# Optimization experiments

Hardware: AMD Instinct MI355X
Metric: run time of the kernel (lower is better)

The kernel has to match this reference:

```python
import jax, jax.numpy as jnp
import numpy as np
import math

B, NH, SQ, HD = 4, 32, 512, 128
MLEN = 3584


def setup_inputs() -> dict:
    key = jax.random.key(0)
    k1, k2, k3, k4 = jax.random.split(key, 4)
    q = jax.random.normal(k1, (B, NH, SQ, HD), dtype=jnp.float32)
    k = jax.random.normal(k2, (B, NH, SQ, HD), dtype=jnp.float32)
    v = jax.random.normal(k3, (B, NH, SQ, HD), dtype=jnp.float32)
    mem = jax.random.normal(k4, (B, MLEN, 2 * NH * HD), dtype=jnp.float32)
    mask = jnp.ones((B, 1, SQ, MLEN + SQ), dtype=jnp.float32)
    return {"q": q, "k": k, "v": v, "mask": mask, "mem": mem}


def reference(q, k, v, mask, mem):
    b, nh, sq, hd = k.shape
    mlen = mem.shape[1]
    # cache_kv: stack (k,v) -> (2,b,nh,sq,hd), permute -> (b,sq,2,nh,hd), flatten
    cache_kv = jnp.stack((k, v)).transpose(1, 3, 0, 2, 4).reshape(b, sq, 2 * nh * hd)
    # split cached mem into memk/memv: (b,mlen,2,nh,hd) -> (2,b,nh,mlen,hd)
    mem_r = mem.reshape(b, mlen, 2, nh, hd).transpose(2, 0, 3, 1, 4)
    k_full = jnp.concatenate([mem_r[0], k], axis=2)  # [b,nh,mlen+sq,hd]
    v_full = jnp.concatenate([mem_r[1], v], axis=2)
    scale = 1.0 / math.sqrt(hd)
    scores = jnp.einsum("bhqd,bhkd->bhqk", q * scale, k_full)
    # standard_attention general mask path (mask.shape[-2] != 1)
    scores = scores * mask - 10000.0 * (1.0 - mask)
    probs = jax.nn.softmax(scores, axis=-1)
    context = jnp.einsum("bhqk,bhkd->bhqd", probs, v_full)
    return context, cache_kv
```

## Files before the change

### kernel.cpp

```cpp
#include <hip/hip_runtime.h>

#define B_ 4
#define NH_ 32
#define SQ_ 512
#define HD_ 128
#define MLEN_ 3584
#define KT_ 4096
#define QB_ 256
#define KB_ 64
#define NTILE_ 64
#define MEMTILES_ 56

typedef float f32x4 __attribute__((ext_vector_type(4)));
typedef short s16x8 __attribute__((ext_vector_type(8)));

__device__ __forceinline__ f32x4 MFMA16(s16x8 a, s16x8 b, f32x4 c) {
    return __builtin_amdgcn_mfma_f32_16x16x32_bf16(a, b, c, 0, 0, 0);
}

__device__ __forceinline__ s16x8 cvt8(float4 a, float4 b, float sc) {
    union { s16x8 v; __bf16 h[8]; } u;
    u.h[0] = (__bf16)(a.x * sc); u.h[1] = (__bf16)(a.y * sc);
    u.h[2] = (__bf16)(a.z * sc); u.h[3] = (__bf16)(a.w * sc);
    u.h[4] = (__bf16)(b.x * sc); u.h[5] = (__bf16)(b.y * sc);
    u.h[6] = (__bf16)(b.z * sc); u.h[7] = (__bf16)(b.w * sc);
    return u.v;
}

__launch_bounds__(512, 2)
__global__ void attn_kernel(const float* __restrict__ q, const float* __restrict__ k,
                            const float* __restrict__ v, const float* __restrict__ mask,
                            const float* __restrict__ mem, float* __restrict__ ctx)
{
    __shared__ __bf16 Klds[KB_ * HD_];
    __shared__ __bf16 Vt[HD_ * KB_];
    __shared__ __bf16 Plds[8 * 32 * KB_];

    const int tid  = threadIdx.x;
    const int lane = tid & 63;
    const int w    = tid >> 6;
    const int l15  = lane & 15;
    const int l4   = lane >> 4;
    const int xv   = (lane & 7) << 4;

    const int qt   = blockIdx.x >> 7;
    const int pair = blockIdx.x & 127;
    const int b    = pair >> 5;
    const int h    = pair & 31;
    const int q0   = qt * QB_;

    const float scale = 0.088388347648318447f;
    s16x8 qf[2][4];
    {
        const float* qbase = q + (((size_t)(b * NH_ + h)) * SQ_ + q0 + w * 32 + l15) * HD_;
        #pragma unroll
        for (int m = 0; m < 2; ++m) {
            #pragma unroll
            for (int kc = 0; kc < 4; ++kc) {
                const float* p = qbase + (size_t)m * 16 * HD_ + kc * 32 + l4 * 8;
                float4 a = *(const float4*)p;
                float4 c = *(const float4*)(p + 4);
                qf[m][kc] = cvt8(a, c, scale);
            }
        }
    }

    f32x4 acc[2][8];
    #pragma unroll
    for (int m = 0; m < 2; ++m)
        #pragma unroll
        for (int n = 0; n < 8; ++n)
            acc[m][n] = (f32x4){0.f, 0.f, 0.f, 0.f};

    float mrun[2][4], lrun[2][4];
    #pragma unroll
    for (int m = 0; m < 2; ++m)
        #pragma unroll
        for (int i = 0; i < 4; ++i) { mrun[m][i] = -3.0e38f; lrun[m][i] = 0.f; }

    const float* maskbase = mask + ((size_t)b * SQ_ + q0 + w * 32 + l4 * 4) * KT_;

    for (int t = 0; t < NTILE_; ++t) {
        const int kv0 = t * KB_;
        const float *srcK, *srcV;
        int rstride;
        if (t < MEMTILES_) {
            const float* mrow = mem + ((size_t)b * MLEN_ + kv0) * (2 * NH_ * HD_) + h * HD_;
            srcK = mrow;
            srcV = mrow + NH_ * HD_;
            rstride = 2 * NH_ * HD_;
        } else {
            size_t off = (((size_t)b * NH_ + h) * SQ_ + (kv0 - MLEN_)) * HD_;
            srcK = k + off;
            srcV = v + off;
            rstride = HD_;
        }

        __syncthreads();

        #pragma unroll
        for (int it = 0; it < 2; ++it) {
            int idx = tid + it * 512;
            int row = idx >> 4, cg = idx & 15;
            const float* p = srcK + (size_t)row * rstride + cg * 8;
            float4 a = *(const float4*)p;
            float4 c = *(const float4*)(p + 4);
            s16x8 vv = cvt8(a, c, 1.0f);
            int byte = row * 256 + ((cg * 16) ^ ((row & 7) << 4));
            *(s16x8*)((char*)Klds + byte) = vv;
        }
        #pragma unroll
        for (int it = 0; it < 2; ++it) {
            int idx = tid + it * 512;
            int hd = idx & 127, kvb = idx >> 7;
            const float* p = srcV + (size_t)(kvb * 8) * rstride + hd;
            union { s16x8 v; __bf16 hh[8]; } u;
            #pragma unroll
            for (int j = 0; j < 8; ++j) u.hh[j] = (__bf16)p[(size_t)j * rstride];
            int byte = hd * 128 + ((kvb * 16) ^ ((hd & 7) << 4));
            *(s16x8*)((char*)Vt + byte) = u.v;
        }

        __syncthreads();

        f32x4 sa[2][4];
        #pragma unroll
        for (int m = 0; m < 2; ++m)
            #pragma unroll
            for (int n = 0; n < 4; ++n)
                sa[m][n] = (f32x4){0.f, 0.f, 0.f, 0.f};
        #pragma unroll
        for (int n = 0; n < 4; ++n) {
            #pragma unroll
            for (int kc = 0; kc < 4; ++kc) {
                s16x8 kf = *(const s16x8*)((const char*)Klds +
                            (n * 16 + l15) * 256 + (((kc * 4 + l4) * 16) ^ xv));
                sa[0][n] = MFMA16(qf[0][kc], kf, sa[0][n]);
                sa[1][n] = MFMA16(qf[1][kc], kf, sa[1][n]);
            }
        }

        #pragma unroll
        for (int m = 0; m < 2; ++m) {
            #pragma unroll
            for (int i = 0; i < 4; ++i) {
                const float* mp = maskbase + (size_t)(m * 16 + i) * KT_ + kv0 + l15;
                float mv0 = mp[0], mv1 = mp[16], mv2 = mp[32], mv3 = mp[48];
                sa[m][0][i] = fmaf(mv0, sa[m][0][i] + 10000.f, -10000.f);
                sa[m][1][i] = fmaf(mv1, sa[m][1][i] + 10000.f, -10000.f);
                sa[m][2][i] = fmaf(mv2, sa[m][2][i] + 10000.f, -10000.f);
                sa[m][3][i] = fmaf(mv3, sa[m][3][i] + 10000.f, -10000.f);

                float rm = fmaxf(fmaxf(sa[m][0][i], sa[m][1][i]),
                                 fmaxf(sa[m][2][i], sa[m][3][i]));
                rm = fmaxf(rm, __shfl_xor(rm, 1));
                rm = fmaxf(rm, __shfl_xor(rm, 2));
                rm = fmaxf(rm, __shfl_xor(rm, 4));
                rm = fmaxf(rm, __shfl_xor(rm, 8));

                float om = mrun[m][i];
                float nm = fmaxf(om, rm);
                float al = __expf(om - nm);
                mrun[m][i] = nm;

                float rs = 0.f;
                #pragma unroll
                for (int n = 0; n < 4; ++n) {
                    float pe = __expf(sa[m][n][i] - nm);
                    sa[m][n][i] = pe;
                    rs += pe;
                }
                rs += __shfl_xor(rs, 1);
                rs += __shfl_xor(rs, 2);
                rs += __shfl_xor(rs, 4);
                rs += __shfl_xor(rs, 8);
                lrun[m][i] = lrun[m][i] * al + rs;

                #pragma unroll
                for (int nn = 0; nn < 8; ++nn) acc[m][nn][i] *= al;
            }
        }

        __bf16* pw = &Plds[w * (32 * KB_)];
        #pragma unroll
        for (int m = 0; m < 2; ++m)
            #pragma unroll
            for (int n = 0; n < 4; ++n)
                #pragma unroll
                for (int i = 0; i < 4; ++i) {
                    int row = m * 16 + l4 * 4 + i;
                    int col = n * 16 + l15;
                    int byte = row * 128 + ((col * 2) ^ ((row & 7) << 4));
                    *(__bf16*)((char*)pw + byte) = (__bf16)sa[m][n][i];
                }

        s16x8 pf[2][2];
        #pragma unroll
        for (int m = 0; m < 2; ++m)
            #pragma unroll
            for (int kt = 0; kt < 2; ++kt)
                pf[m][kt] = *(const s16x8*)((const char*)pw +
                              (m * 16 + l15) * 128 + ((kt * 64 + l4 * 16) ^ xv));
        #pragma unroll
        for (int nn = 0; nn < 8; ++nn) {
            s16x8 vf0 = *(const s16x8*)((const char*)Vt +
                          (nn * 16 + l15) * 128 + ((l4 * 16) ^ xv));
            s16x8 vf1 = *(const s16x8*)((const char*)Vt +
                          (nn * 16 + l15) * 128 + ((64 + l4 * 16) ^ xv));
            #pragma unroll
            for (int m = 0; m < 2; ++m) {
                acc[m][nn] = MFMA16(pf[m][0], vf0, acc[m][nn]);
                acc[m][nn] = MFMA16(pf[m][1], vf1, acc[m][nn]);
            }
        }
    }

    float* obase = ctx + (((size_t)(b * NH_ + h)) * SQ_ + q0 + w * 32 + l4 * 4) * HD_ + l15;
    #pragma unroll
    for (int m = 0; m < 2; ++m)
        #pragma unroll
        for (int i = 0; i < 4; ++i) {
            float inv = 1.f / lrun[m][i];
            #pragma unroll
            for (int nn = 0; nn < 8; ++nn)
                obase[(size_t)(m * 16 + i) * HD_ + nn * 16] = acc[m][nn][i] * inv;
        }
}

__global__ void cachekv_kernel(const float* __restrict__ k, const float* __restrict__ v,
                               float* __restrict__ out)
{
    size_t i = ((size_t)blockIdx.x * 256 + threadIdx.x) * 4;
    unsigned f = (unsigned)i;
    unsigned d    = f & 127;
    unsigned hh   = (f >> 7) & 31;
    unsigned part = (f >> 12) & 1;
    unsigned s    = (f >> 13) & 511;
    unsigned bb   = f >> 22;
    const float* src = (part ? v : k) + (((size_t)(bb * 32u + hh)) * 512u + s) * 128u + d;
    *(float4*)(out + i) = *(const float4*)src;
}

extern "C" void kernel_launch(void* const* d_in, const int* in_sizes, int n_in,
                              void* d_out, int out_size, void* d_ws, size_t ws_size,
                              hipStream_t stream) {
    const float* q    = (const float*)d_in[0];
    const float* k    = (const float*)d_in[1];
    const float* v    = (const float*)d_in[2];
    const float* mask = (const float*)d_in[3];
    const float* mem  = (const float*)d_in[4];
    float* out = (float*)d_out;

    attn_kernel<<<dim3(B_ * NH_ * (SQ_ / QB_)), dim3(512), 0, stream>>>(q, k, v, mask, mem, out);

    const int ctx_elems = B_ * NH_ * SQ_ * HD_;
    const int ckv_elems = B_ * SQ_ * 2 * NH_ * HD_;
    cachekv_kernel<<<dim3(ckv_elems / 4 / 256), dim3(256), 0, stream>>>(k, v, out + ctx_elems);
    (void)in_sizes; (void)n_in; (void)out_size; (void)d_ws; (void)ws_size;
}
```

Measured before the change: 382.9 us.

## Software-pipeline K/V tile loads into registers and prefetch mask values

Global loads for the next K/V tile are issued into registers before computing the current tile, and converted and written to LDS after the compute with an extra barrier. Mask values for the current tile are also loaded at the top of the iteration. The aim is to hide global memory latency behind the MFMA and softmax work. The cost is higher register pressure (about 40 more floats per thread plus mask prefetch), which could reduce occupancy or cause spills.

Result: slower. 409.4 us (+6.9%).

```diff
diff --git a/kernel.cpp b/kernel.cpp
--- a/kernel.cpp
+++ b/kernel.cpp
@@ -80,7 +80,13 @@
 
     const float* maskbase = mask + ((size_t)b * SQ_ + q0 + w * 32 + l4 * 4) * KT_;
 
-    for (int t = 0; t < NTILE_; ++t) {
+    const int krow = tid >> 4,  kcg  = tid & 15;
+    const int vhd  = tid & 127, vkvb = tid >> 7;
+
+    float4 kpa[2], kpb[2];
+    float  vpre[2][8];
+
+    auto issueKV = [&](int t) {
         const int kv0 = t * KB_;
         const float *srcK, *srcV;
         int rstride;
@@ -95,31 +101,55 @@
             srcV = v + off;
             rstride = HD_;
         }
-
-        __syncthreads();
-
-        #pragma unroll
-        for (int it = 0; it < 2; ++it) {
-            int idx = tid + it * 512;
-            int row = idx >> 4, cg = idx & 15;
-            const float* p = srcK + (size_t)row * rstride + cg * 8;
-            float4 a = *(const float4*)p;
-            float4 c = *(const float4*)(p + 4);
-            s16x8 vv = cvt8(a, c, 1.0f);
-            int byte = row * 256 + ((cg * 16) ^ ((row & 7) << 4));
+        #pragma unroll
+        for (int it = 0; it < 2; ++it) {
+            const float* p = srcK + (size_t)(krow + it * 32) * rstride + kcg * 8;
+            kpa[it] = *(const float4*)p;
+            kpb[it] = *(const float4*)(p + 4);
+        }
+        #pragma unroll
+        for (int it = 0; it < 2; ++it) {
+            const float* p = srcV + (size_t)((vkvb + it * 4) * 8) * rstride + vhd;
+            #pragma unroll
+            for (int j = 0; j < 8; ++j) vpre[it][j] = p[(size_t)j * rstride];
+        }
+    };
+    auto writeKV = [&]() {
+        #pragma unroll
+        for (int it = 0; it < 2; ++it) {
+            int row = krow + it * 32;
+            s16x8 vv = cvt8(kpa[it], kpb[it], 1.0f);
+            int byte = row * 256 + ((kcg * 16) ^ ((row & 7) << 4));
             *(s16x8*)((char*)Klds + byte) = vv;
         }
         #pragma unroll
         for (int it = 0; it < 2; ++it) {
-            int idx = tid + it * 512;
-            int hd = idx & 127, kvb = idx >> 7;
-            const float* p = srcV + (size_t)(kvb * 8) * rstride + hd;
+            int kvb = vkvb + it * 4;
             union { s16x8 v; __bf16 hh[8]; } u;
             #pragma unroll
-            for (int j = 0; j < 8; ++j) u.hh[j] = (__bf16)p[(size_t)j * rstride];
-            int byte = hd * 128 + ((kvb * 16) ^ ((hd & 7) << 4));
+            for (int j = 0; j < 8; ++j) u.hh[j] = (__bf16)vpre[it][j];
+            int byte = vhd * 128 + ((kvb * 16) ^ ((vhd & 7) << 4));
             *(s16x8*)((char*)Vt + byte) = u.v;
         }
+    };
+
+    issueKV(0);
+    writeKV();
+
+    for (int t = 0; t < NTILE_; ++t) {
+        const int kv0 = t * KB_;
+
+        float mpre[2][4][4];
+        #pragma unroll
+        for (int m = 0; m < 2; ++m)
+            #pragma unroll
+            for (int i = 0; i < 4; ++i) {
+                const float* mp = maskbase + (size_t)(m * 16 + i) * KT_ + kv0 + l15;
+                #pragma unroll
+                for (int n = 0; n < 4; ++n) mpre[m][i][n] = mp[n * 16];
+            }
+
+        if (t + 1 < NTILE_) issueKV(t + 1);
 
         __syncthreads();
 
@@ -144,12 +174,10 @@
         for (int m = 0; m < 2; ++m) {
             #pragma unroll
             for (int i = 0; i < 4; ++i) {
-                const float* mp = maskbase + (size_t)(m * 16 + i) * KT_ + kv0 + l15;
-                float mv0 = mp[0], mv1 = mp[16], mv2 = mp[32], mv3 = mp[48];
-                sa[m][0][i] = fmaf(mv0, sa[m][0][i] + 10000.f, -10000.f);
-                sa[m][1][i] = fmaf(mv1, sa[m][1][i] + 10000.f, -10000.f);
-                sa[m][2][i] = fmaf(mv2, sa[m][2][i] + 10000.f, -10000.f);
-                sa[m][3][i] = fmaf(mv3, sa[m][3][i] + 10000.f, -10000.f);
+                sa[m][0][i] = fmaf(mpre[m][i][0], sa[m][0][i] + 10000.f, -10000.f);
+                sa[m][1][i] = fmaf(mpre[m][i][1], sa[m][1][i] + 10000.f, -10000.f);
+                sa[m][2][i] = fmaf(mpre[m][i][2], sa[m][2][i] + 10000.f, -10000.f);
+                sa[m][3][i] = fmaf(mpre[m][i][3], sa[m][3][i] + 10000.f, -10000.f);
 
                 float rm = fmaxf(fmaxf(sa[m][0][i], sa[m][1][i]),
                                  fmaxf(sa[m][2][i], sa[m][3][i]));
@@ -213,6 +241,10 @@
                 acc[m][nn] = MFMA16(pf[m][1], vf1, acc[m][nn]);
             }
         }
+
+        __syncthreads();
+
+        if (t + 1 < NTILE_) writeKV();
     }
 
     float* obase = ctx + (((size_t)(b * NH_ + h)) * SQ_ + q0 + w * 32 + l4 * 4) * HD_ + l15;
```

## Halve query tile per block, raise occupancy, and prefetch mask before barrier

Applied to the files above, without the earlier changes.

Cuts the query tile from 256 to 128 rows, so each wave owns 16 query rows instead of 32. This halves the per-thread accumulator, softmax-state and Q-fragment registers and allows 4 blocks per CU. Mask values for a tile are now loaded before the barrier so their latency overlaps the K/V staging. The cost is that every K/V tile, including the large mem cache, is converted and staged by twice as many blocks, which doubles global K/V reads unless L2 or the last-level cache absorbs them.

After: 346.3 us. -9.5%, faster.

```diff
diff --git a/kernel.cpp b/kernel.cpp
--- a/kernel.cpp
+++ b/kernel.cpp
@@ -6,7 +6,7 @@
 #define HD_ 128
 #define MLEN_ 3584
 #define KT_ 4096
-#define QB_ 256
+#define QB_ 128
 #define KB_ 64
 #define NTILE_ 64
 #define MEMTILES_ 56
@@ -18,23 +18,23 @@
     return __builtin_amdgcn_mfma_f32_16x16x32_bf16(a, b, c, 0, 0, 0);
 }
 
-__device__ __forceinline__ s16x8 cvt8(float4 a, float4 b, float sc) {
+__device__ __forceinline__ s16x8 cvt8(float4 a, float4 b) {
     union { s16x8 v; __bf16 h[8]; } u;
-    u.h[0] = (__bf16)(a.x * sc); u.h[1] = (__bf16)(a.y * sc);
-    u.h[2] = (__bf16)(a.z * sc); u.h[3] = (__bf16)(a.w * sc);
-    u.h[4] = (__bf16)(b.x * sc); u.h[5] = (__bf16)(b.y * sc);
-    u.h[6] = (__bf16)(b.z * sc); u.h[7] = (__bf16)(b.w * sc);
+    u.h[0] = (__bf16)a.x; u.h[1] = (__bf16)a.y;
+    u.h[2] = (__bf16)a.z; u.h[3] = (__bf16)a.w;
+    u.h[4] = (__bf16)b.x; u.h[5] = (__bf16)b.y;
+    u.h[6] = (__bf16)b.z; u.h[7] = (__bf16)b.w;
     return u.v;
 }
 
-__launch_bounds__(512, 2)
+__launch_bounds__(512, 4)
 __global__ void attn_kernel(const float* __restrict__ q, const float* __restrict__ k,
                             const float* __restrict__ v, const float* __restrict__ mask,
                             const float* __restrict__ mem, float* __restrict__ ctx)
 {
     __shared__ __bf16 Klds[KB_ * HD_];
     __shared__ __bf16 Vt[HD_ * KB_];
-    __shared__ __bf16 Plds[8 * 32 * KB_];
+    __shared__ __bf16 Plds[8 * 16 * KB_];
 
     const int tid  = threadIdx.x;
     const int lane = tid & 63;
@@ -50,35 +50,29 @@
     const int q0   = qt * QB_;
 
     const float scale = 0.088388347648318447f;
-    s16x8 qf[2][4];
+    s16x8 qf[4];
     {
-        const float* qbase = q + (((size_t)(b * NH_ + h)) * SQ_ + q0 + w * 32 + l15) * HD_;
-        #pragma unroll
-        for (int m = 0; m < 2; ++m) {
-            #pragma unroll
-            for (int kc = 0; kc < 4; ++kc) {
-                const float* p = qbase + (size_t)m * 16 * HD_ + kc * 32 + l4 * 8;
-                float4 a = *(const float4*)p;
-                float4 c = *(const float4*)(p + 4);
-                qf[m][kc] = cvt8(a, c, scale);
-            }
+        const float* qbase = q + (((size_t)(b * NH_ + h)) * SQ_ + q0 + w * 16 + l15) * HD_;
+        #pragma unroll
+        for (int kc = 0; kc < 4; ++kc) {
+            const float* p = qbase + kc * 32 + l4 * 8;
+            float4 a = *(const float4*)p;
+            float4 c = *(const float4*)(p + 4);
+            a.x *= scale; a.y *= scale; a.z *= scale; a.w *= scale;
+            c.x *= scale; c.y *= scale; c.z *= scale; c.w *= scale;
+            qf[kc] = cvt8(a, c);
         }
     }
 
-    f32x4 acc[2][8];
+    f32x4 acc[8];
     #pragma unroll
-    for (int m = 0; m < 2; ++m)
-        #pragma unroll
-        for (int n = 0; n < 8; ++n)
-            acc[m][n] = (f32x4){0.f, 0.f, 0.f, 0.f};
-
-    float mrun[2][4], lrun[2][4];
+    for (int n = 0; n < 8; ++n) acc[n] = (f32x4){0.f, 0.f, 0.f, 0.f};
+
+    float mrun[4], lrun[4];
     #pragma unroll
-    for (int m = 0; m < 2; ++m)
-        #pragma unroll
-        for (int i = 0; i < 4; ++i) { mrun[m][i] = -3.0e38f; lrun[m][i] = 0.f; }
-
-    const float* maskbase = mask + ((size_t)b * SQ_ + q0 + w * 32 + l4 * 4) * KT_;
+    for (int i = 0; i < 4; ++i) { mrun[i] = -3.0e38f; lrun[i] = 0.f; }
+
+    const float* maskbase = mask + ((size_t)b * SQ_ + q0 + w * 16 + l4 * 4) * KT_;
 
     for (int t = 0; t < NTILE_; ++t) {
         const int kv0 = t * KB_;
@@ -105,7 +99,7 @@
             const float* p = srcK + (size_t)row * rstride + cg * 8;
             float4 a = *(const float4*)p;
             float4 c = *(const float4*)(p + 4);
-            s16x8 vv = cvt8(a, c, 1.0f);
+            s16x8 vv = cvt8(a, c);
             int byte = row * 256 + ((cg * 16) ^ ((row & 7) << 4));
             *(s16x8*)((char*)Klds + byte) = vv;
         }
@@ -121,110 +115,99 @@
             *(s16x8*)((char*)Vt + byte) = u.v;
         }
 
+        float mpre[4][4];
+        #pragma unroll
+        for (int i = 0; i < 4; ++i) {
+            const float* mp = maskbase + (size_t)i * KT_ + kv0 + l15;
+            #pragma unroll
+            for (int n = 0; n < 4; ++n) mpre[i][n] = mp[n * 16];
+        }
+
         __syncthreads();
 
-        f32x4 sa[2][4];
-        #pragma unroll
-        for (int m = 0; m < 2; ++m)
-            #pragma unroll
-            for (int n = 0; n < 4; ++n)
-                sa[m][n] = (f32x4){0.f, 0.f, 0.f, 0.f};
+        f32x4 sa[4];
+        #pragma unroll
+        for (int n = 0; n < 4; ++n) sa[n] = (f32x4){0.f, 0.f, 0.f, 0.f};
         #pragma unroll
         for (int n = 0; n < 4; ++n) {
             #pragma unroll
             for (int kc = 0; kc < 4; ++kc) {
                 s16x8 kf = *(const s16x8*)((const char*)Klds +
                             (n * 16 + l15) * 256 + (((kc * 4 + l4) * 16) ^ xv));
-                sa[0][n] = MFMA16(qf[0][kc], kf, sa[0][n]);
-                sa[1][n] = MFMA16(qf[1][kc], kf, sa[1][n]);
+                sa[n] = MFMA16(qf[kc], kf, sa[n]);
             }
         }
 
         #pragma unroll
-        for (int m = 0; m < 2; ++m) {
+        for (int i = 0; i < 4; ++i) {
+            sa[0][i] = fmaf(mpre[i][0], sa[0][i] + 10000.f, -10000.f);
+            sa[1][i] = fmaf(mpre[i][1], sa[1][i] + 10000.f, -10000.f);
+            sa[2][i] = fmaf(mpre[i][2], sa[2][i] + 10000.f, -10000.f);
+            sa[3][i] = fmaf(mpre[i][3], sa[3][i] + 10000.f, -10000.f);
+
+            float rm = fmaxf(fmaxf(sa[0][i], sa[1][i]), fmaxf(sa[2][i], sa[3][i]));
+            rm = fmaxf(rm, __shfl_xor(rm, 1));
+            rm = fmaxf(rm, __shfl_xor(rm, 2));
+            rm = fmaxf(rm, __shfl_xor(rm, 4));
+            rm = fmaxf(rm, __shfl_xor(rm, 8));
+
+            float om = mrun[i];
+            float nm = fmaxf(om, rm);
+            float al = __expf(om - nm);
+            mrun[i] = nm;
+
+            float rs = 0.f;
+            #pragma unroll
+            for (int n = 0; n < 4; ++n) {
+                float pe = __expf(sa[n][i] - nm);
+                sa[n][i] = pe;
+                rs += pe;
+            }
+            rs += __shfl_xor(rs, 1);
+            rs += __shfl_xor(rs, 2);
+            rs += __shfl_xor(rs, 4);
+            rs += __shfl_xor(rs, 8);
+            lrun[i] = lrun[i] * al + rs;
+
+            #pragma unroll
+            for (int nn = 0; nn < 8; ++nn) acc[nn][i] *= al;
+        }
+
+        __bf16* pw = &Plds[w * (16 * KB_)];
+        #pragma unroll
+        for (int n = 0; n < 4; ++n)
             #pragma unroll
             for (int i = 0; i < 4; ++i) {
-                const float* mp = maskbase + (size_t)(m * 16 + i) * KT_ + kv0 + l15;
-                float mv0 = mp[0], mv1 = mp[16], mv2 = mp[32], mv3 = mp[48];
-                sa[m][0][i] = fmaf(mv0, sa[m][0][i] + 10000.f, -10000.f);
-                sa[m][1][i] = fmaf(mv1, sa[m][1][i] + 10000.f, -10000.f);
-                sa[m][2][i] = fmaf(mv2, sa[m][2][i] + 10000.f, -10000.f);
-                sa[m][3][i] = fmaf(mv3, sa[m][3][i] + 10000.f, -10000.f);
-
-                float rm = fmaxf(fmaxf(sa[m][0][i], sa[m][1][i]),
-                                 fmaxf(sa[m][2][i], sa[m][3][i]));
-                rm = fmaxf(rm, __shfl_xor(rm, 1));
-                rm = fmaxf(rm, __shfl_xor(rm, 2));
-                rm = fmaxf(rm, __shfl_xor(rm, 4));
-                rm = fmaxf(rm, __shfl_xor(rm, 8));
-
-                float om = mrun[m][i];
-                float nm = fmaxf(om, rm);
-                float al = __expf(om - nm);
-                mrun[m][i] = nm;
-
-                float rs = 0.f;
-                #pragma unroll
-                for (int n = 0; n < 4; ++n) {
-                    float pe = __expf(sa[m][n][i] - nm);
-                    sa[m][n][i] = pe;
-                    rs += pe;
-                }
-                rs += __shfl_xor(rs, 1);
-                rs += __shfl_xor(rs, 2);
-                rs += __shfl_xor(rs, 4);
-                rs += __shfl_xor(rs, 8);
-                lrun[m][i] = lrun[m][i] * al + rs;
-
-                #pragma unroll
-                for (int nn = 0; nn < 8; ++nn) acc[m][nn][i] *= al;
+                int row = l4 * 4 + i;
+                int col = n * 16 + l15;
+                int byte = row * 128 + ((col * 2) ^ ((row & 7) << 4));
+                *(__bf16*)((char*)pw + byte) = (__bf16)sa[n][i];
             }
-        }
-
-        __bf16* pw = &Plds[w * (32 * KB_)];
-        #pragma unroll
-        for (int m = 0; m < 2; ++m)
-            #pragma unroll
-            for (int n = 0; n < 4; ++n)
-                #pragma unroll
-                for (int i = 0; i < 4; ++i) {
-                    int row = m * 16 + l4 * 4 + i;
-                    int col = n * 16 + l15;
-                    int byte = row * 128 + ((col * 2) ^ ((row & 7) << 4));
-                    *(__bf16*)((char*)pw + byte) = (__bf16)sa[m][n][i];
-                }
-
-        s16x8 pf[2][2];
-        #pragma unroll
-        for (int m = 0; m < 2; ++m)
-            #pragma unroll
-            for (int kt = 0; kt < 2; ++kt)
-                pf[m][kt] = *(const s16x8*)((const char*)pw +
-                              (m * 16 + l15) * 128 + ((kt * 64 + l4 * 16) ^ xv));
+
+        s16x8 pf[2];
+        #pragma unroll
+        for (int kt = 0; kt < 2; ++kt)
+            pf[kt] = *(const s16x8*)((const char*)pw +
+                          l15 * 128 + ((kt * 64 + l4 * 16) ^ xv));
         #pragma unroll
         for (int nn = 0; nn < 8; ++nn) {
             s16x8 vf0 = *(const s16x8*)((const char*)Vt +
                           (nn * 16 + l15) * 128 + ((l4 * 16) ^ xv));
             s16x8 vf1 = *(const s16x8*)((const char*)Vt +
                           (nn * 16 + l15) * 128 + ((64 + l4 * 16) ^ xv));
-            #pragma unroll
-            for (int m = 0; m < 2; ++m) {
-                acc[m][nn] = MFMA16(pf[m][0], vf0, acc[m][nn]);
-                acc[m][nn] = MFMA16(pf[m][1], vf1, acc[m][nn]);
-            }
+            acc[nn] = MFMA16(pf[0], vf0, acc[nn]);
+            acc[nn] = MFMA16(pf[1], vf1, acc[nn]);
         }
     }
 
-    float* obase = ctx + (((size_t)(b * NH_ + h)) * SQ_ + q0 + w * 32 + l4 * 4) * HD_ + l15;
+    float* obase = ctx + (((size_t)(b * NH_ + h)) * SQ_ + q0 + w * 16 + l4 * 4) * HD_ + l15;
     #pragma unroll
-    for (int m = 0; m < 2; ++m)
-        #pragma unroll
-        for (int i = 0; i < 4; ++i) {
-            float inv = 1.f / lrun[m][i];
-            #pragma unroll
-            for (int nn = 0; nn < 8; ++nn)
-                obase[(size_t)(m * 16 + i) * HD_ + nn * 16] = acc[m][nn][i] * inv;
-        }
+    for (int i = 0; i < 4; ++i) {
+        float inv = 1.f / lrun[i];
+        #pragma unroll
+        for (int nn = 0; nn < 8; ++nn)
+            obase[(size_t)i * HD_ + nn * 16] = acc[nn][i] * inv;
+    }
 }
 
 __global__ void cachekv_kernel(const float* __restrict__ k, const float* __restrict__ v,
```
